# Performance work log

Measured on AMD Instinct MI355X. Metric: run time of the kernel, lower is better.

## Reference

```python
import jax, jax.numpy as jnp
import numpy as np

# GCN ('gcn' variant): avg-pooled adjacency, per-step linear + propagation + ReLU,
# final output projection, then select the target (first) node of each block.
# The original builds a dense block-diagonal (B*n, B*n) adjacency via torch.block_diag;
# since off-block entries are exactly zero, this is mathematically identical to
# batched per-block matmuls, which is what we do here.

B, N_NODES, D_IN, D_HID, D_OUT, STEPS = 256, 512, 256, 256, 128, 3


def setup_inputs() -> dict:
    key = jax.random.key(0)
    ks = jax.random.split(key, 6)
    xavier = lambda k, shp: jax.random.normal(k, shp, jnp.float32) * np.sqrt(2.0 / (shp[0] + shp[1]))
    feat = jax.random.normal(ks[0], (B * N_NODES, D_IN), jnp.float32)
    raw_adj = jax.random.uniform(ks[1], (B, N_NODES, N_NODES), jnp.float32)
    W0 = xavier(ks[2], (D_IN, D_HID))
    W1 = xavier(ks[3], (D_HID, D_HID))
    W2 = xavier(ks[4], (D_HID, D_HID))
    Wout = xavier(ks[5], (D_HID, D_OUT))
    return {"feat": feat, "raw_adj": raw_adj, "W0": W0, "W1": W1, "W2": W2, "Wout": Wout}


def reference(feat, raw_adj, W0, W1, W2, Wout):
    b, n, _ = raw_adj.shape
    d = feat.shape[1]
    Xb = feat.reshape(b, n, d)  # block view of feat

    # avg_pooling: row-normalize adjacency by the sum over columns whose
    # feature rows are nonzero (block-diagonal => per-block computation).
    nz = (jnp.linalg.norm(Xb, axis=2) > 0).astype(raw_adj.dtype)  # (b, n)
    row_sum = jnp.einsum('bij,bj->bi', raw_adj, nz)               # (b, n)
    row_sum = jnp.where(row_sum == 0, 1.0, row_sum)
    adj = raw_adj / row_sum[:, :, None]

    X = Xb
    for W in (W0, W1, W2):
        Z = jnp.einsum('bnd,dh->bnh', X, W)      # per-step linear (no bias)
        X = jax.nn.relu(jnp.einsum('bij,bjh->bih', adj, Z))  # propagate + ReLU
    out = jnp.einsum('bnh,ho->bno', X, Wout)     # output layer
    # X[ids] with ids = [0, n, 2n, ...] == first node of each block
    return out[:, 0, :]
```

## Files before the change

### kernel.cpp

```cpp
#include <hip/hip_runtime.h>


typedef __attribute__((ext_vector_type(8))) short short8;
typedef __attribute__((ext_vector_type(4))) float f32x4;

__device__ __forceinline__ unsigned short f2bf(float x) {
  unsigned u = __float_as_uint(x);
  unsigned r = u + 0x7fffu + ((u >> 16) & 1u);
  return (unsigned short)(r >> 16);
}
__device__ __forceinline__ float bf2f(unsigned short b) {
  return __uint_as_float(((unsigned)b) << 16);
}
__device__ __forceinline__ unsigned pkbf(float lo, float hi) {
  unsigned r;
  asm("v_cvt_pk_bf16_f32 %0, %1, %2" : "=v"(r) : "v"(lo), "v"(hi));
  return r;
}

#define GLDS(g, l) __builtin_amdgcn_global_load_lds( \
    (const __attribute__((address_space(1))) void*)(g), \
    (__attribute__((address_space(3))) void*)(l), 16, 0, 0)

__device__ __forceinline__ int swz2048(int bid) { return (bid & 7) * 256 + (bid >> 3); }

__global__ void k_wconv(const float* __restrict__ W0, const float* __restrict__ W1,
                        unsigned short* __restrict__ Wt) {
  int s = blockIdx.x >> 8;
  int n = blockIdx.x & 255;
  int k = threadIdx.x;
  const float* W = s ? W1 : W0;
  Wt[(size_t)s * 65536 + n * 256 + k] = f2bf(W[(size_t)k * 256 + n]);
}

__global__ void k_adj(const float* __restrict__ adj, const float* __restrict__ nz,
                      unsigned short* __restrict__ adjN) {
  int row = blockIdx.x * 4 + (threadIdx.x >> 6);
  int lane = threadIdx.x & 63;
  int b = row >> 9;
  const float4* src = (const float4*)(adj + (size_t)row * 512);
  float4 a0 = src[lane * 2], a1 = src[lane * 2 + 1];
  const float4* nzp = (const float4*)(nz + (size_t)b * 512);
  float4 z0 = nzp[lane * 2], z1 = nzp[lane * 2 + 1];
  float s = a0.x * z0.x + a0.y * z0.y + a0.z * z0.z + a0.w * z0.w
          + a1.x * z1.x + a1.y * z1.y + a1.z * z1.z + a1.w * z1.w;
#pragma unroll
  for (int off = 1; off < 64; off <<= 1) s += __shfl_xor(s, off);
  float inv = 1.f / ((s == 0.f) ? 1.f : s);
  uint4 p;
  p.x = pkbf(a0.x * inv, a0.y * inv);
  p.y = pkbf(a0.z * inv, a0.w * inv);
  p.z = pkbf(a1.x * inv, a1.y * inv);
  p.w = pkbf(a1.z * inv, a1.w * inv);
  ((uint4*)(adjN + (size_t)row * 512))[lane] = p;
}

__device__ __forceinline__ void gemm_dbuf(
    const char* Ag, int ldaB, const char* Bg, int ldbB, int nkt,
    char* lds, f32x4 acc[4][4], int wm, int wn, int lane, int tid) {
  char* ldsA = lds;
  char* ldsB = lds + 32768;
#define STAGE_AB(KT, BUF) do {                                           \
    _Pragma("unroll")                                                    \
    for (int q = 0; q < 4; ++q) {                                        \
      int P = (q * 256 + tid) * 16;                                      \
      int L = P ^ (((P >> 7) & 7) << 4);                                 \
      int row = L >> 7, cb = L & 127;                                    \
      GLDS(Ag + (size_t)row * ldaB + (KT) * 128 + cb,                    \
           ldsA + (BUF) * 16384 + P);                                    \
      GLDS(Bg + (size_t)row * ldbB + (KT) * 128 + cb,                    \
           ldsB + (BUF) * 16384 + P);                                    \
    } } while (0)
  STAGE_AB(0, 0);
  __syncthreads();
  for (int kt = 0; kt < nkt; ++kt) {
    int cur = kt & 1;
    if (kt + 1 < nkt) STAGE_AB(kt + 1, cur ^ 1);
#pragma unroll
    for (int ks = 0; ks < 2; ++ks) {
      short8 af[4], bfr[4];
      int c = ks * 64 + ((lane >> 4) << 4);
#pragma unroll
      for (int m = 0; m < 4; ++m) {
        int row = wm * 64 + m * 16 + (lane & 15);
        af[m] = *(const short8*)(ldsA + cur * 16384 + ((row * 128 + c) ^ ((row & 7) << 4)));
      }
#pragma unroll
      for (int n = 0; n < 4; ++n) {
        int row = wn * 64 + n * 16 + (lane & 15);
        bfr[n] = *(const short8*)(ldsB + cur * 16384 + ((row * 128 + c) ^ ((row & 7) << 4)));
      }
#pragma unroll
      for (int m = 0; m < 4; ++m)
#pragma unroll
        for (int n = 0; n < 4; ++n)
          acc[m][n] = __builtin_amdgcn_mfma_f32_16x16x32_bf16(af[m], bfr[n], acc[m][n], 0, 0, 0);
    }
    __syncthreads();
  }
#undef STAGE_AB
}

__global__ __launch_bounds__(256) void k_lin0(const float* __restrict__ feat,
                                              const unsigned short* __restrict__ Wt,
                                              unsigned short* __restrict__ Zt,
                                              float* __restrict__ nzOut) {
  __shared__ char ldsA[32768];
  __shared__ char ldsB[32768];
  int tid = threadIdx.x, lane = tid & 63, wid = tid >> 6;
  int wm = wid >> 1, wn = wid & 1;
  int tile = swz2048(blockIdx.x);
  int tm = tile >> 1, tn = tile & 1;
  const float* Ag = feat + (size_t)tm * 128 * 256;
  const char* Bg = (const char*)(Wt + (size_t)tn * 128 * 256);
  int r = tid >> 1, hk = tid & 1;
  const float* myrow = Ag + (size_t)r * 256 + hk * 32;
  float ssq = 0.f;
  f32x4 acc[4][4];
#pragma unroll
  for (int m = 0; m < 4; ++m)
#pragma unroll
    for (int n = 0; n < 4; ++n) { f32x4 z = {0.f, 0.f, 0.f, 0.f}; acc[m][n] = z; }

#define L0_STAGE_B(KT, BUF) do {                                         \
    _Pragma("unroll")                                                    \
    for (int q = 0; q < 4; ++q) {                                        \
      int P = (q * 256 + tid) * 16;                                      \
      int L = P ^ (((P >> 7) & 7) << 4);                                 \
      int row = L >> 7, cb = L & 127;                                    \
      GLDS(Bg + (size_t)row * 512 + (KT) * 128 + cb,                     \
           ldsB + (BUF) * 16384 + P);                                    \
    } } while (0)
#define L0_LOAD_A(KT) do {                                               \
    _Pragma("unroll")                                                    \
    for (int q = 0; q < 8; ++q)                                          \
      fA[q] = ((const float4*)(myrow + (KT) * 64))[q];                   \
    } while (0)
#define L0_WRITE_A(BUF) do {                                             \
    _Pragma("unroll")                                                    \
    for (int q = 0; q < 8; ++q)                                          \
      ssq += fA[q].x * fA[q].x + fA[q].y * fA[q].y                       \
           + fA[q].z * fA[q].z + fA[q].w * fA[q].w;                      \
    _Pragma("unroll")                                                    \
    for (int q = 0; q < 4; ++q) {                                        \
      uint4 w;                                                           \
      w.x = pkbf(fA[2 * q].x, fA[2 * q].y);                              \
      w.y = pkbf(fA[2 * q].z, fA[2 * q].w);                              \
      w.z = pkbf(fA[2 * q + 1].x, fA[2 * q + 1].y);                      \
      w.w = pkbf(fA[2 * q + 1].z, fA[2 * q + 1].w);                      \
      int cb = hk * 64 + q * 16;                                         \
      *(uint4*)(ldsA + (BUF) * 16384 +                                   \
                ((r * 128 + cb) ^ ((r & 7) << 4))) = w;                  \
    } } while (0)

  float4 fA[8];
  L0_LOAD_A(0);
  L0_STAGE_B(0, 0);
  L0_WRITE_A(0);
  __syncthreads();

#pragma unroll
  for (int kt = 0; kt < 4; ++kt) {
    int cur = kt & 1;
    if (kt < 3) {
      L0_LOAD_A(kt + 1);
      L0_STAGE_B(kt + 1, cur ^ 1);
    }
#pragma unroll
    for (int ks = 0; ks < 2; ++ks) {
      short8 af[4], bfr[4];
      int c = ks * 64 + ((lane >> 4) << 4);
#pragma unroll
      for (int m = 0; m < 4; ++m) {
        int row = wm * 64 + m * 16 + (lane & 15);
        af[m] = *(const short8*)(ldsA + cur * 16384 + ((row * 128 + c) ^ ((row & 7) << 4)));
      }
#pragma unroll
      for (int n = 0; n < 4; ++n) {
        int row = wn * 64 + n * 16 + (lane & 15);
        bfr[n] = *(const short8*)(ldsB + cur * 16384 + ((row * 128 + c) ^ ((row & 7) << 4)));
      }
#pragma unroll
      for (int m = 0; m < 4; ++m)
#pragma unroll
        for (int n = 0; n < 4; ++n)
          acc[m][n] = __builtin_amdgcn_mfma_f32_16x16x32_bf16(af[m], bfr[n], acc[m][n], 0, 0, 0);
    }
    if (kt < 3) L0_WRITE_A(cur ^ 1);
    __syncthreads();
  }
#undef L0_STAGE_B
#undef L0_LOAD_A
#undef L0_WRITE_A

  float tot = ssq + __shfl_xor(ssq, 1);
  if (hk == 0 && tn == 0) nzOut[(size_t)tm * 128 + r] = (tot > 0.f) ? 1.f : 0.f;

  int b = tm >> 2;
  int node_base = ((tm & 3) * 128) + wm * 64;
  int h_base = tn * 128 + wn * 64;
#pragma unroll
  for (int m = 0; m < 4; ++m) {
    int node = node_base + m * 16 + ((lane >> 4) << 2);
#pragma unroll
    for (int n = 0; n < 4; ++n) {
      int h = h_base + n * 16 + (lane & 15);
      f32x4 v = acc[m][n];
      ushort4 p;
      p.x = f2bf(v[0]); p.y = f2bf(v[1]); p.z = f2bf(v[2]); p.w = f2bf(v[3]);
      *(ushort4*)(Zt + ((size_t)b * 256 + h) * 512 + node) = p;
    }
  }
}

__global__ __launch_bounds__(256) void k_prop(const unsigned short* __restrict__ adjN,
                                              const unsigned short* __restrict__ Zt,
                                              unsigned short* __restrict__ Xout) {
  __shared__ char lds[65536];
  int tid = threadIdx.x, lane = tid & 63, wid = tid >> 6;
  int wm = wid >> 1, wn = wid & 1;
  int tile = swz2048(blockIdx.x);
  int b = tile >> 3, tm = (tile >> 1) & 3, tn = tile & 1;
  const char* Ag = (const char*)(adjN + ((size_t)b * 512 + tm * 128) * 512);
  const char* Bg = (const char*)(Zt + ((size_t)b * 256 + tn * 128) * 512);
  f32x4 acc[4][4];
#pragma unroll
  for (int m = 0; m < 4; ++m)
#pragma unroll
    for (int n = 0; n < 4; ++n) { f32x4 z = {0.f, 0.f, 0.f, 0.f}; acc[m][n] = z; }
  gemm_dbuf(Ag, 1024, Bg, 1024, 8, lds, acc, wm, wn, lane, tid);
  int node_base = tm * 128 + wm * 64;
  int h_base = tn * 128 + wn * 64;
#pragma unroll
  for (int m = 0; m < 4; ++m) {
    int node = node_base + m * 16 + ((lane >> 4) << 2);
#pragma unroll
    for (int n = 0; n < 4; ++n) {
      int h = h_base + n * 16 + (lane & 15);
#pragma unroll
      for (int r = 0; r < 4; ++r) {
        float v = acc[m][n][r];
        v = v > 0.f ? v : 0.f;
        Xout[((size_t)b * 512 + node + r) * 256 + h] = f2bf(v);
      }
    }
  }
}

__global__ __launch_bounds__(256) void k_propy(const unsigned short* __restrict__ adjN,
                                               const unsigned short* __restrict__ Zt,
                                               float* __restrict__ yws) {
  __shared__ char lds[65536];
  __shared__ float ybuf[2][128];
  int tid = threadIdx.x, lane = tid & 63, wid = tid >> 6;
  int wm = wid >> 1, wn = wid & 1;
  int tile = swz2048(blockIdx.x);
  int b = tile >> 3, tm = (tile >> 1) & 3, tn = tile & 1;
  const char* Ag = (const char*)(adjN + ((size_t)b * 512 + tm * 128) * 512);
  const char* Bg = (const char*)(Zt + ((size_t)b * 256 + tn * 128) * 512);
  f32x4 acc[4][4];
#pragma unroll
  for (int m = 0; m < 4; ++m)
#pragma unroll
    for (int n = 0; n < 4; ++n) { f32x4 z = {0.f, 0.f, 0.f, 0.f}; acc[m][n] = z; }
  gemm_dbuf(Ag, 1024, Bg, 1024, 8, lds, acc, wm, wn, lane, tid);

  int kq = lane >> 4, r0 = lane & 15;
  float yp[4] = {0.f, 0.f, 0.f, 0.f};
#pragma unroll
  for (int m = 0; m < 4; ++m) {
    int node = tm * 128 + wm * 64 + m * 16 + kq * 4;
    ushort4 a4 = *(const ushort4*)(adjN + (size_t)b * 262144 + node);
    float a[4] = {bf2f(a4.x), bf2f(a4.y), bf2f(a4.z), bf2f(a4.w)};
#pragma unroll
    for (int n = 0; n < 4; ++n)
#pragma unroll
      for (int r = 0; r < 4; ++r) {
        float v = acc[m][n][r];
        v = v > 0.f ? v : 0.f;
        yp[n] += v * a[r];
      }
  }
#pragma unroll
  for (int n = 0; n < 4; ++n) {
    yp[n] += __shfl_xor(yp[n], 16);
    yp[n] += __shfl_xor(yp[n], 32);
  }
  if (lane < 16) {
#pragma unroll
    for (int n = 0; n < 4; ++n) ybuf[wm][wn * 64 + n * 16 + lane] = yp[n];
  }
  __syncthreads();
  if (tid < 128)
    yws[((size_t)b * 4 + tm) * 256 + tn * 128 + tid] = ybuf[0][tid] + ybuf[1][tid];
}

__global__ __launch_bounds__(256) void k_linear(const unsigned short* __restrict__ X,
                                                const unsigned short* __restrict__ Wt,
                                                unsigned short* __restrict__ Zt) {
  __shared__ char lds[65536];
  int tid = threadIdx.x, lane = tid & 63, wid = tid >> 6;
  int wm = wid >> 1, wn = wid & 1;
  int tile = swz2048(blockIdx.x);
  int tm = tile >> 1, tn = tile & 1;
  const char* Ag = (const char*)(X + (size_t)tm * 128 * 256);
  const char* Bg = (const char*)(Wt + (size_t)tn * 128 * 256);
  f32x4 acc[4][4];
#pragma unroll
  for (int m = 0; m < 4; ++m)
#pragma unroll
    for (int n = 0; n < 4; ++n) { f32x4 z = {0.f, 0.f, 0.f, 0.f}; acc[m][n] = z; }
  gemm_dbuf(Ag, 512, Bg, 512, 4, lds, acc, wm, wn, lane, tid);
  int b = tm >> 2;
  int node_base = ((tm & 3) * 128) + wm * 64;
  int h_base = tn * 128 + wn * 64;
#pragma unroll
  for (int m = 0; m < 4; ++m) {
    int node = node_base + m * 16 + ((lane >> 4) << 2);
#pragma unroll
    for (int n = 0; n < 4; ++n) {
      int h = h_base + n * 16 + (lane & 15);
      f32x4 v = acc[m][n];
      ushort4 p;
      p.x = f2bf(v[0]); p.y = f2bf(v[1]); p.z = f2bf(v[2]); p.w = f2bf(v[3]);
      *(ushort4*)(Zt + ((size_t)b * 256 + h) * 512 + node) = p;
    }
  }
}

__global__ __launch_bounds__(256) void k_tail(const float* __restrict__ yws,
                                              const float* __restrict__ W2,
                                              const float* __restrict__ Wout,
                                              float* __restrict__ out) {
  __shared__ float y[256];
  __shared__ float x3[256];
  int b = blockIdx.x, tid = threadIdx.x;
  const float* w = yws + (size_t)b * 1024;
  y[tid] = w[tid] + w[256 + tid] + w[512 + tid] + w[768 + tid];
  __syncthreads();
  {
    float s = 0.f;
    for (int k = 0; k < 256; ++k) s += y[k] * W2[(size_t)k * 256 + tid];
    x3[tid] = s > 0.f ? s : 0.f;
  }
  __syncthreads();
  if (tid < 128) {
    float s = 0.f;
    for (int h = 0; h < 256; ++h) s += x3[h] * Wout[(size_t)h * 128 + tid];
    out[(size_t)b * 128 + tid] = s;
  }
}

extern "C" void kernel_launch(void* const* d_in, const int* in_sizes, int n_in,
                              void* d_out, int out_size, void* d_ws, size_t ws_size,
                              hipStream_t stream) {
  (void)in_sizes; (void)n_in; (void)out_size; (void)ws_size;
  const float* feat = (const float*)d_in[0];
  const float* adj  = (const float*)d_in[1];
  const float* W0   = (const float*)d_in[2];
  const float* W1   = (const float*)d_in[3];
  const float* W2   = (const float*)d_in[4];
  const float* Wout = (const float*)d_in[5];
  float* out = (float*)d_out;

  char* ws = (char*)d_ws;
  unsigned short* adjN = (unsigned short*)(ws);
  unsigned short* Xbuf = (unsigned short*)(ws + 134217728);
  unsigned short* Zt   = (unsigned short*)(ws + 201326592);
  float* nzbuf         = (float*)(ws + 268435456);
  unsigned short* Wt   = (unsigned short*)(ws + 268959744);
  float* yws           = (float*)(ws + 269221888);

  k_wconv<<<512, 256, 0, stream>>>(W0, W1, Wt);
  k_lin0<<<2048, 256, 0, stream>>>(feat, Wt, Zt, nzbuf);
  k_adj<<<32768, 256, 0, stream>>>(adj, nzbuf, adjN);
  k_prop<<<2048, 256, 0, stream>>>(adjN, Zt, Xbuf);
  k_linear<<<2048, 256, 0, stream>>>(Xbuf, Wt + 65536, Zt);
  k_propy<<<2048, 256, 0, stream>>>(adjN, Zt, yws);
  k_tail<<<256, 256, 0, stream>>>(yws, W2, Wout, out);
}
```

Baseline: 313.3 us.

## Pipeline GEMM loads with explicit vmcnt waits and coalesce lin0 A loads

Replaces the __syncthreads double-buffer loop with a two-tile prefetch: both stages are issued up front and each iteration waits with s_waitcnt vmcnt(8) before a raw s_barrier. The next-but-one tile is issued only after the compute barrier, so global-to-LDS loads overlap MFMA work and the full drain every iteration goes away. Separately, k_lin0 now reads A so that 16 consecutive threads cover a contiguous row segment, giving coalesced float4 loads, with the per-row norm reduced over 16-lane shuffles. The hand-counted vmcnt depends on each STAGE_AB issuing exactly 8 loads per thread, which is fragile if the compiler reorders or splits them.

```diff
diff --git a/kernel.cpp b/kernel.cpp
--- a/kernel.cpp
+++ b/kernel.cpp
@@ -55,7 +55,7 @@
   ((uint4*)(adjN + (size_t)row * 512))[lane] = p;
 }
 
-__device__ __forceinline__ void gemm_dbuf(
+__device__ __forceinline__ void gemm_cnt(
     const char* Ag, int ldaB, const char* Bg, int ldbB, int nkt,
     char* lds, f32x4 acc[4][4], int wm, int wn, int lane, int tid) {
   char* ldsA = lds;
@@ -72,10 +72,14 @@
            ldsB + (BUF) * 16384 + P);                                    \
     } } while (0)
   STAGE_AB(0, 0);
-  __syncthreads();
+  STAGE_AB(1, 1);
+#pragma unroll
   for (int kt = 0; kt < nkt; ++kt) {
     int cur = kt & 1;
-    if (kt + 1 < nkt) STAGE_AB(kt + 1, cur ^ 1);
+    if (kt + 1 < nkt) asm volatile("s_waitcnt vmcnt(8)" ::: "memory");
+    else              asm volatile("s_waitcnt vmcnt(0)" ::: "memory");
+    __builtin_amdgcn_s_barrier();
+    __builtin_amdgcn_sched_barrier(0);
 #pragma unroll
     for (int ks = 0; ks < 2; ++ks) {
       short8 af[4], bfr[4];
@@ -96,7 +100,9 @@
         for (int n = 0; n < 4; ++n)
           acc[m][n] = __builtin_amdgcn_mfma_f32_16x16x32_bf16(af[m], bfr[n], acc[m][n], 0, 0, 0);
     }
-    __syncthreads();
+    __builtin_amdgcn_sched_barrier(0);
+    __builtin_amdgcn_s_barrier();
+    if (kt + 2 < nkt) STAGE_AB(kt + 2, cur);
   }
 #undef STAGE_AB
 }
@@ -113,9 +119,10 @@
   int tm = tile >> 1, tn = tile & 1;
   const float* Ag = feat + (size_t)tm * 128 * 256;
   const char* Bg = (const char*)(Wt + (size_t)tn * 128 * 256);
-  int r = tid >> 1, hk = tid & 1;
-  const float* myrow = Ag + (size_t)r * 256 + hk * 32;
-  float ssq = 0.f;
+  const float* myA = Ag + (size_t)(tid >> 4) * 256 + (tid & 15) * 4;
+  int arow = tid >> 4;
+  float ss[8] = {0.f, 0.f, 0.f, 0.f, 0.f, 0.f, 0.f, 0.f};
+  float4 fA[8];
   f32x4 acc[4][4];
 #pragma unroll
   for (int m = 0; m < 4; ++m)
@@ -134,26 +141,21 @@
 #define L0_LOAD_A(KT) do {                                               \
     _Pragma("unroll")                                                    \
     for (int q = 0; q < 8; ++q)                                          \
-      fA[q] = ((const float4*)(myrow + (KT) * 64))[q];                   \
+      fA[q] = *(const float4*)(myA + q * 4096 + (KT) * 64);              \
     } while (0)
 #define L0_WRITE_A(BUF) do {                                             \
     _Pragma("unroll")                                                    \
-    for (int q = 0; q < 8; ++q)                                          \
-      ssq += fA[q].x * fA[q].x + fA[q].y * fA[q].y                       \
-           + fA[q].z * fA[q].z + fA[q].w * fA[q].w;                      \
-    _Pragma("unroll")                                                    \
-    for (int q = 0; q < 4; ++q) {                                        \
-      uint4 w;                                                           \
-      w.x = pkbf(fA[2 * q].x, fA[2 * q].y);                              \
-      w.y = pkbf(fA[2 * q].z, fA[2 * q].w);                              \
-      w.z = pkbf(fA[2 * q + 1].x, fA[2 * q + 1].y);                      \
-      w.w = pkbf(fA[2 * q + 1].z, fA[2 * q + 1].w);                      \
-      int cb = hk * 64 + q * 16;                                         \
-      *(uint4*)(ldsA + (BUF) * 16384 +                                   \
-                ((r * 128 + cb) ^ ((r & 7) << 4))) = w;                  \
+    for (int q = 0; q < 8; ++q) {                                        \
+      ss[q] += fA[q].x * fA[q].x + fA[q].y * fA[q].y                     \
+             + fA[q].z * fA[q].z + fA[q].w * fA[q].w;                    \
+      uint2 w;                                                           \
+      w.x = pkbf(fA[q].x, fA[q].y);                                      \
+      w.y = pkbf(fA[q].z, fA[q].w);                                      \
+      int row = q * 16 + arow;                                           \
+      int byte = (row * 128 + (tid & 15) * 8) ^ ((row & 7) << 4);        \
+      *(uint2*)(ldsA + (BUF) * 16384 + byte) = w;                        \
     } } while (0)
 
-  float4 fA[8];
   L0_LOAD_A(0);
   L0_STAGE_B(0, 0);
   L0_WRITE_A(0);
@@ -193,8 +195,18 @@
 #undef L0_LOAD_A
 #undef L0_WRITE_A
 
-  float tot = ssq + __shfl_xor(ssq, 1);
-  if (hk == 0 && tn == 0) nzOut[(size_t)tm * 128 + r] = (tot > 0.f) ? 1.f : 0.f;
+  if (tn == 0) {
+#pragma unroll
+    for (int q = 0; q < 8; ++q) {
+      float v = ss[q];
+      v += __shfl_xor(v, 1);
+      v += __shfl_xor(v, 2);
+      v += __shfl_xor(v, 4);
+      v += __shfl_xor(v, 8);
+      if ((lane & 15) == 0)
+        nzOut[(size_t)tm * 128 + q * 16 + arow] = (v > 0.f) ? 1.f : 0.f;
+    }
+  }
 
   int b = tm >> 2;
   int node_base = ((tm & 3) * 128) + wm * 64;
@@ -228,7 +240,7 @@
   for (int m = 0; m < 4; ++m)
 #pragma unroll
     for (int n = 0; n < 4; ++n) { f32x4 z = {0.f, 0.f, 0.f, 0.f}; acc[m][n] = z; }
-  gemm_dbuf(Ag, 1024, Bg, 1024, 8, lds, acc, wm, wn, lane, tid);
+  gemm_cnt(Ag, 1024, Bg, 1024, 8, lds, acc, wm, wn, lane, tid);
   int node_base = tm * 128 + wm * 64;
   int h_base = tn * 128 + wn * 64;
 #pragma unroll
@@ -263,7 +275,7 @@
   for (int m = 0; m < 4; ++m)
 #pragma unroll
     for (int n = 0; n < 4; ++n) { f32x4 z = {0.f, 0.f, 0.f, 0.f}; acc[m][n] = z; }
-  gemm_dbuf(Ag, 1024, Bg, 1024, 8, lds, acc, wm, wn, lane, tid);
+  gemm_cnt(Ag, 1024, Bg, 1024, 8, lds, acc, wm, wn, lane, tid);
 
   int kq = lane >> 4, r0 = lane & 15;
   float yp[4] = {0.f, 0.f, 0.f, 0.f};
@@ -310,7 +322,7 @@
   for (int m = 0; m < 4; ++m)
 #pragma unroll
     for (int n = 0; n < 4; ++n) { f32x4 z = {0.f, 0.f, 0.f, 0.f}; acc[m][n] = z; }
-  gemm_dbuf(Ag, 512, Bg, 512, 4, lds, acc, wm, wn, lane, tid);
+  gemm_cnt(Ag, 512, Bg, 512, 4, lds, acc, wm, wn, lane, tid);
   int b = tm >> 2;
   int node_base = ((tm & 3) * 128) + wm * 64;
   int h_base = tn * 128 + wn * 64;
```

New measurement: 330.9 us. 1.06x slower.
